# Kernel optimization log

Hardware: AMD Instinct MI355X
Metric: run time of the kernel (lower is better)

The kernel has to match this reference:

```python
import jax, jax.numpy as jnp
import numpy as np

EMBED = 1024
HEADS = 16
HEAD_DIM = EMBED // HEADS  # 64


def setup_inputs() -> dict:
    key = jax.random.key(0)
    k0, k1, k2, k3, k4 = jax.random.split(key, 5)
    scale = 1.0 / np.sqrt(EMBED)
    return {
        "input_tensor": jax.random.normal(k0, (2, 2048, EMBED), dtype=jnp.float32),
        "qkv_w": jax.random.normal(k1, (EMBED, 3 * EMBED), dtype=jnp.float32) * scale,
        "qkv_b": jax.random.normal(k2, (3 * EMBED,), dtype=jnp.float32) * 0.02,
        "out_w": jax.random.normal(k3, (EMBED, EMBED), dtype=jnp.float32) * scale,
        "out_b": jax.random.normal(k4, (EMBED,), dtype=jnp.float32) * 0.02,
    }


def reference(input_tensor, qkv_w, qkv_b, out_w, out_b):
    B, S, _ = input_tensor.shape
    qkv = input_tensor @ qkv_w + qkv_b  # [B,S,3E]
    q, k, v = jnp.split(qkv, 3, axis=-1)
    # [B,S,E] -> [B,H,S,D]
    def to_heads(t):
        return t.reshape(B, S, HEADS, HEAD_DIM).transpose(0, 2, 1, 3)
    q, k, v = to_heads(q), to_heads(k), to_heads(v)
    scores = jnp.einsum("bhqd,bhkd->bhqk", q, k) / jnp.sqrt(jnp.float32(HEAD_DIM))
    probs = jax.nn.softmax(scores, axis=-1)  # dropout p=0 -> identity
    attn = jnp.einsum("bhqk,bhkd->bhqd", probs, v)
    attn = attn.transpose(0, 2, 1, 3).reshape(B, S, EMBED)
    return attn @ out_w + out_b
```

## Files before the change

kernel.cpp:

```cpp
#include <hip/hip_runtime.h>
#include <stdint.h>

typedef short short4v __attribute__((ext_vector_type(4)));
typedef short short8  __attribute__((ext_vector_type(8)));
typedef float f32x4   __attribute__((ext_vector_type(4)));
typedef unsigned int u32x2 __attribute__((ext_vector_type(2)));

#define S_LEN 2048
#define NB    2
#define NH    16
#define HD    64
#define EMB   1024
#define TOK   (NB * S_LEN)
#define QKV_N (3 * EMB)

#define GLD16(gp, lp) __builtin_amdgcn_global_load_lds( \
    (const __attribute__((address_space(1))) void*)(gp), \
    (__attribute__((address_space(3))) void*)(lp), 16, 0, 0)

static __device__ __forceinline__ short f2bf(float f) {
    unsigned int x = __float_as_uint(f);
    unsigned int r = (x + 0x7fffu + ((x >> 16) & 1u)) >> 16;
    return (short)(r & 0xffffu);
}

static __device__ __forceinline__ f32x4 mfma16(short8 a, short8 b, f32x4 c) {
    return __builtin_amdgcn_mfma_f32_16x16x32_bf16(a, b, c, 0, 0, 0);
}

__global__ __launch_bounds__(256) void cvt_f32_bf16(const float* __restrict__ in,
                                                    short* __restrict__ out, int n) {
    int i = (blockIdx.x * 256 + threadIdx.x) * 4;
    if (i < n) {
        float4 v = *reinterpret_cast<const float4*>(in + i);
        short4v o;
        o.x = f2bf(v.x); o.y = f2bf(v.y); o.z = f2bf(v.z); o.w = f2bf(v.w);
        *reinterpret_cast<short4v*>(out + i) = o;
    }
}

__global__ __launch_bounds__(256) void transpose_cvt(const float* __restrict__ w,
                                                     short* __restrict__ wt,
                                                     int K, int N) {
    __shared__ float tile[32][33];
    int tx = threadIdx.x & 31, ty = threadIdx.x >> 5;
    int c0 = blockIdx.x * 32, r0 = blockIdx.y * 32;
    #pragma unroll
    for (int j = 0; j < 4; j++)
        tile[ty + j * 8][tx] = w[(long)(r0 + ty + j * 8) * N + c0 + tx];
    __syncthreads();
    #pragma unroll
    for (int j = 0; j < 4; j++)
        wt[(long)(c0 + ty + j * 8) * K + r0 + tx] = f2bf(tile[tx][ty + j * 8]);
}

__global__ __launch_bounds__(256) void vtrans(const short* __restrict__ v,
                                              short* __restrict__ vt) {
    __shared__ short t[32][33];
    int tx = threadIdx.x & 31, ty = threadIdx.x >> 5;
    int s0 = blockIdx.x * 32, d0 = blockIdx.y * 32, bh = blockIdx.z;
    const long base = (long)bh * S_LEN * HD;
    #pragma unroll
    for (int j = 0; j < 4; j++)
        t[ty + j * 8][tx] = v[base + (long)(s0 + ty + j * 8) * HD + d0 + tx];
    __syncthreads();
    #pragma unroll
    for (int j = 0; j < 4; j++)
        vt[base + (long)(d0 + ty + j * 8) * S_LEN + s0 + tx] = t[tx][ty + j * 8];
}

template <int EPI>
__global__ __launch_bounds__(256) void gemm_bf16(
    const short* __restrict__ A, const short* __restrict__ BT,
    const float* __restrict__ bias,
    short* __restrict__ q_ws, short* __restrict__ k_ws, short* __restrict__ v_ws,
    float* __restrict__ outf, int M, int N, int K) {
    __shared__ __align__(16) short As[128 * 64];
    __shared__ __align__(16) short Bs[128 * 64];
    const int tid = threadIdx.x;
    const int lane = tid & 63, wave = tid >> 6;
    const int wm = wave >> 1, wn = wave & 1;
    const int l15 = lane & 15, lhi = lane >> 4;
    const int bm = blockIdx.y, bn = blockIdx.x;

    const short* gA[4]; const short* gB[4]; short* lA[4]; short* lB[4];
    #pragma unroll
    for (int i = 0; i < 4; i++) {
        int inst = wave * 4 + i;
        int row  = inst * 8 + (lane >> 3);
        int c    = lane & 7, cp = c ^ (row & 7);
        gA[i] = A  + (long)(bm * 128 + row) * K + cp * 8;
        gB[i] = BT + (long)(bn * 128 + row) * K + cp * 8;
        lA[i] = As + inst * 512;
        lB[i] = Bs + inst * 512;
    }

    f32x4 acc[4][4] = {};
    for (int kt = 0; kt < K; kt += 64) {
        #pragma unroll
        for (int i = 0; i < 4; i++) { GLD16(gA[i] + kt, lA[i]); GLD16(gB[i] + kt, lB[i]); }
        __syncthreads();
        #pragma unroll
        for (int ks = 0; ks < 2; ks++) {
            short8 af[4], bfr[4];
            #pragma unroll
            for (int m = 0; m < 4; m++) {
                int row = wm * 64 + m * 16 + l15;
                int cp  = (ks * 4 + lhi) ^ (row & 7);
                af[m] = *(const short8*)(As + row * 64 + cp * 8);
            }
            #pragma unroll
            for (int n = 0; n < 4; n++) {
                int row = wn * 64 + n * 16 + l15;
                int cp  = (ks * 4 + lhi) ^ (row & 7);
                bfr[n] = *(const short8*)(Bs + row * 64 + cp * 8);
            }
            #pragma unroll
            for (int m = 0; m < 4; m++)
                #pragma unroll
                for (int n = 0; n < 4; n++)
                    acc[m][n] = mfma16(af[m], bfr[n], acc[m][n]);
        }
        __syncthreads();
    }

    if (EPI == 0) {
        const int part = bn >> 3;
        short* dst = part == 0 ? q_ws : (part == 1 ? k_ws : v_ws);
        #pragma unroll
        for (int m = 0; m < 4; m++) {
            const int row0 = bm * 128 + wm * 64 + m * 16 + lhi * 4;
            #pragma unroll
            for (int n = 0; n < 4; n++) {
                const int col = bn * 128 + wn * 64 + n * 16 + l15;
                const float bv = bias[col];
                const int nn = col & 1023, h = nn >> 6, d = nn & 63;
                #pragma unroll
                for (int r = 0; r < 4; r++) {
                    const int rr = row0 + r, b = rr >> 11, s = rr & 2047;
                    dst[((long)(b * NH + h) * S_LEN + s) * HD + d] =
                        f2bf(acc[m][n][r] + bv);
                }
            }
        }
    } else {
        #pragma unroll
        for (int m = 0; m < 4; m++) {
            const int row0 = bm * 128 + wm * 64 + m * 16 + lhi * 4;
            #pragma unroll
            for (int n = 0; n < 4; n++) {
                const int col = bn * 128 + wn * 64 + n * 16 + l15;
                const float bv = bias[col];
                #pragma unroll
                for (int r = 0; r < 4; r++)
                    outf[(long)(row0 + r) * N + col] = acc[m][n][r] + bv;
            }
        }
    }
}

__global__ __launch_bounds__(256) void attn_fwd(const short* __restrict__ Qg,
                                                const short* __restrict__ Kg,
                                                const short* __restrict__ Vtg,
                                                short* __restrict__ Og) {
    __shared__ __align__(16) short Ks[64 * 64];
    __shared__ __align__(16) short Vs[64 * 64];
    __shared__ __align__(16) short Pl[4][16][72];
    const int tid = threadIdx.x, lane = tid & 63, wave = tid >> 6;
    const int l15 = lane & 15, lhi = lane >> 4;
    const int bh = blockIdx.y, qt = blockIdx.x;
    const int q0 = qt * 64 + wave * 16;
    const long kbase = (long)bh * S_LEN * HD;
    const long vbase = (long)bh * HD * S_LEN;

    short8 qf[2];
    #pragma unroll
    for (int ks2 = 0; ks2 < 2; ks2++)
        qf[ks2] = *(const short8*)&Qg[kbase + (long)(q0 + l15) * HD + ks2 * 32 + lhi * 8];

    const short* gK[2]; const short* gV[2]; short* lK[2]; short* lV[2];
    #pragma unroll
    for (int i = 0; i < 2; i++) {
        int inst = wave * 2 + i;
        int row  = inst * 8 + (lane >> 3);
        int c    = lane & 7, cp = c ^ (row & 7);
        gK[i] = Kg  + kbase + (long)row * HD + cp * 8;
        gV[i] = Vtg + vbase + (long)row * S_LEN + cp * 8;
        lK[i] = Ks + inst * 512;
        lV[i] = Vs + inst * 512;
    }

    f32x4 accO[4] = {};
    float ms = -1e30f, lp = 0.f;
    const float C2 = 0.18033688f;

    for (int kv = 0; kv < S_LEN; kv += 64) {
        #pragma unroll
        for (int i = 0; i < 2; i++) { GLD16(gK[i] + (long)kv * HD, lK[i]); GLD16(gV[i] + kv, lV[i]); }
        __syncthreads();

        f32x4 accS[4];
        #pragma unroll
        for (int ksub = 0; ksub < 4; ksub++) {
            f32x4 z = {0.f, 0.f, 0.f, 0.f};
            #pragma unroll
            for (int ks2 = 0; ks2 < 2; ks2++) {
                int row = ksub * 16 + l15;
                int cp  = (ks2 * 4 + lhi) ^ (row & 7);
                short8 kf = *(const short8*)(Ks + row * 64 + cp * 8);
                z = mfma16(kf, qf[ks2], z);
            }
            accS[ksub] = z;
        }

        f32x4 mx = accS[0];
        #pragma unroll
        for (int ksub = 1; ksub < 4; ksub++)
            #pragma unroll
            for (int r = 0; r < 4; r++) mx[r] = fmaxf(mx[r], accS[ksub][r]);
        float m4 = fmaxf(fmaxf(mx[0], mx[1]), fmaxf(mx[2], mx[3]));
        m4 = fmaxf(m4, __shfl_xor(m4, 16));
        m4 = fmaxf(m4, __shfl_xor(m4, 32));
        float msc = m4 * C2;

        if (__any(msc > ms + 8.f)) {
            float msn = fmaxf(ms, msc);
            float corr = exp2f(ms - msn);
            ms = msn;
            lp *= corr;
            #pragma unroll
            for (int r = 0; r < 4; r++) {
                float cr = __shfl(corr, lhi * 4 + r);
                #pragma unroll
                for (int ds = 0; ds < 4; ds++) accO[ds][r] *= cr;
            }
        }

        float lsum = 0.f;
        #pragma unroll
        for (int ksub = 0; ksub < 4; ksub++) {
            f32x4 p;
            #pragma unroll
            for (int r = 0; r < 4; r++)
                p[r] = exp2f(fmaf(accS[ksub][r], C2, -ms));
            lsum += (p[0] + p[1]) + (p[2] + p[3]);
            unsigned pa, pb;
            asm("v_cvt_pk_bf16_f32 %0, %1, %2" : "=v"(pa) : "v"(p[0]), "v"(p[1]));
            asm("v_cvt_pk_bf16_f32 %0, %1, %2" : "=v"(pb) : "v"(p[2]), "v"(p[3]));
            u32x2 w; w[0] = pa; w[1] = pb;
            *(u32x2*)(&Pl[wave][l15][ksub * 16 + lhi * 4]) = w;
        }
        lp += lsum;

        #pragma unroll
        for (int ds = 0; ds < 4; ds++) {
            #pragma unroll
            for (int ks2 = 0; ks2 < 2; ks2++) {
                int row = ds * 16 + l15;
                int cp  = (ks2 * 4 + lhi) ^ (row & 7);
                short8 vf = *(const short8*)(Vs + row * 64 + cp * 8);
                short8 pf = *(const short8*)(&Pl[wave][l15][ks2 * 32 + lhi * 8]);
                accO[ds] = mfma16(pf, vf, accO[ds]);
            }
        }
        __syncthreads();
    }

    float L = lp + __shfl_xor(lp, 16);
    L += __shfl_xor(L, 32);
    const int b = bh >> 4, h = bh & 15;
    #pragma unroll
    for (int r = 0; r < 4; r++) {
        float Lr  = __shfl(L, lhi * 4 + r);
        float inv = 1.f / Lr;
        const int s = q0 + lhi * 4 + r;
        #pragma unroll
        for (int ds = 0; ds < 4; ds++)
            Og[((long)(b * S_LEN + s)) * EMB + h * 64 + ds * 16 + l15] =
                f2bf(accO[ds][r] * inv);
    }
}

extern "C" void kernel_launch(void* const* d_in, const int* in_sizes, int n_in,
                              void* d_out, int out_size, void* d_ws, size_t ws_size,
                              hipStream_t stream) {
    const float* x    = (const float*)d_in[0];
    const float* qkvw = (const float*)d_in[1];
    const float* qkvb = (const float*)d_in[2];
    const float* outw = (const float*)d_in[3];
    const float* outb = (const float*)d_in[4];
    float* out = (float*)d_out;

    char* ws = (char*)d_ws;
    size_t off = 0;
    auto alloc = [&](size_t bytes) {
        void* p = ws + off;
        off += (bytes + 255) & ~(size_t)255;
        return p;
    };
    short* xb    = (short*)alloc((size_t)TOK * EMB * 2);
    short* wqkvT = (short*)alloc((size_t)QKV_N * EMB * 2);
    short* owT   = (short*)alloc((size_t)EMB * EMB * 2);
    short* q_ws  = (short*)alloc((size_t)NB * NH * S_LEN * HD * 2);
    short* k_ws  = (short*)alloc((size_t)NB * NH * S_LEN * HD * 2);
    short* v_ws  = (short*)alloc((size_t)NB * NH * S_LEN * HD * 2);
    short* vt_ws = (short*)alloc((size_t)NB * NH * S_LEN * HD * 2);
    short* attn  = (short*)alloc((size_t)TOK * EMB * 2);

    cvt_f32_bf16<<<(TOK * EMB / 4 + 255) / 256, 256, 0, stream>>>(x, xb, TOK * EMB);
    transpose_cvt<<<dim3(QKV_N / 32, EMB / 32), 256, 0, stream>>>(qkvw, wqkvT, EMB, QKV_N);
    transpose_cvt<<<dim3(EMB / 32, EMB / 32), 256, 0, stream>>>(outw, owT, EMB, EMB);

    gemm_bf16<0><<<dim3(QKV_N / 128, TOK / 128), 256, 0, stream>>>(
        xb, wqkvT, qkvb, q_ws, k_ws, v_ws, nullptr, TOK, QKV_N, EMB);

    vtrans<<<dim3(S_LEN / 32, HD / 32, NB * NH), 256, 0, stream>>>(v_ws, vt_ws);

    attn_fwd<<<dim3(S_LEN / 64, NB * NH), 256, 0, stream>>>(q_ws, k_ws, vt_ws, attn);

    gemm_bf16<1><<<dim3(EMB / 128, TOK / 128), 256, 0, stream>>>(
        attn, owT, outb, nullptr, nullptr, nullptr, out, TOK, EMB, EMB);
}
```

Baseline: 231.0 us.

## Double-buffer K/V tiles in attention and swizzle workgroup order

```diff
diff --git a/kernel.cpp b/kernel.cpp
--- a/kernel.cpp
+++ b/kernel.cpp
@@ -163,12 +163,15 @@
                                                 const short* __restrict__ Kg,
                                                 const short* __restrict__ Vtg,
                                                 short* __restrict__ Og) {
-    __shared__ __align__(16) short Ks[64 * 64];
-    __shared__ __align__(16) short Vs[64 * 64];
+    __shared__ __align__(16) short Ks[2][4096];
+    __shared__ __align__(16) short Vs[2][4096];
     __shared__ __align__(16) short Pl[4][16][72];
     const int tid = threadIdx.x, lane = tid & 63, wave = tid >> 6;
     const int l15 = lane & 15, lhi = lane >> 4;
-    const int bh = blockIdx.y, qt = blockIdx.x;
+    const int wg  = blockIdx.x;
+    const int swz = (wg & 7) * 128 + (wg >> 3);
+    const int bh  = swz >> 5;
+    const int qt  = swz & 31;
     const int q0 = qt * 64 + wave * 16;
     const long kbase = (long)bh * S_LEN * HD;
     const long vbase = (long)bh * HD * S_LEN;
@@ -178,46 +181,62 @@
     for (int ks2 = 0; ks2 < 2; ks2++)
         qf[ks2] = *(const short8*)&Qg[kbase + (long)(q0 + l15) * HD + ks2 * 32 + lhi * 8];
 
-    const short* gK[2]; const short* gV[2]; short* lK[2]; short* lV[2];
+    const short* gKp[2]; const short* gVp[2]; int lOff[2];
     #pragma unroll
     for (int i = 0; i < 2; i++) {
         int inst = wave * 2 + i;
         int row  = inst * 8 + (lane >> 3);
-        int c    = lane & 7, cp = c ^ (row & 7);
-        gK[i] = Kg  + kbase + (long)row * HD + cp * 8;
-        gV[i] = Vtg + vbase + (long)row * S_LEN + cp * 8;
-        lK[i] = Ks + inst * 512;
-        lV[i] = Vs + inst * 512;
-    }
+        int cp   = (lane & 7) ^ (row & 7);
+        gKp[i] = Kg  + kbase + (long)row * HD + cp * 8;
+        gVp[i] = Vtg + vbase + (long)row * S_LEN + cp * 8;
+        lOff[i] = inst * 512;
+    }
+
+    int fOff[4][2];
+    #pragma unroll
+    for (int sub = 0; sub < 4; sub++)
+        #pragma unroll
+        for (int ks2 = 0; ks2 < 2; ks2++) {
+            int row = sub * 16 + l15;
+            int cp  = (ks2 * 4 + lhi) ^ (l15 & 7);
+            fOff[sub][ks2] = row * 64 + cp * 8;
+        }
 
     f32x4 accO[4] = {};
     float ms = -1e30f, lp = 0.f;
     const float C2 = 0.18033688f;
 
-    for (int kv = 0; kv < S_LEN; kv += 64) {
-        #pragma unroll
-        for (int i = 0; i < 2; i++) { GLD16(gK[i] + (long)kv * HD, lK[i]); GLD16(gV[i] + kv, lV[i]); }
-        __syncthreads();
-
+    #pragma unroll
+    for (int i = 0; i < 2; i++) { GLD16(gKp[i], &Ks[0][lOff[i]]); GLD16(gVp[i], &Vs[0][lOff[i]]); }
+    __syncthreads();
+
+    const int NT = S_LEN / 64;
+    for (int t = 0; t < NT; t++) {
+        const int cur = t & 1;
+        if (t + 1 < NT) {
+            #pragma unroll
+            for (int i = 0; i < 2; i++) {
+                GLD16(gKp[i] + (long)(t + 1) * 4096, &Ks[cur ^ 1][lOff[i]]);
+                GLD16(gVp[i] + (t + 1) * 64,         &Vs[cur ^ 1][lOff[i]]);
+            }
+        }
         f32x4 accS[4];
         #pragma unroll
-        for (int ksub = 0; ksub < 4; ksub++) {
+        for (int sub = 0; sub < 4; sub++) {
             f32x4 z = {0.f, 0.f, 0.f, 0.f};
             #pragma unroll
             for (int ks2 = 0; ks2 < 2; ks2++) {
-                int row = ksub * 16 + l15;
-                int cp  = (ks2 * 4 + lhi) ^ (row & 7);
-                short8 kf = *(const short8*)(Ks + row * 64 + cp * 8);
+                short8 kf = *(const short8*)&Ks[cur][fOff[sub][ks2]];
                 z = mfma16(kf, qf[ks2], z);
             }
-            accS[ksub] = z;
+            accS[sub] = z;
         }
 
         f32x4 mx = accS[0];
         #pragma unroll
-        for (int ksub = 1; ksub < 4; ksub++)
-            #pragma unroll
-            for (int r = 0; r < 4; r++) mx[r] = fmaxf(mx[r], accS[ksub][r]);
+        for (int sub = 1; sub < 4; sub++)
+            #pragma unroll
+            for (int r = 0; r < 4; r++) mx[r] = fmaxf(mx[r], accS[sub][r]);
         float m4 = fmaxf(fmaxf(mx[0], mx[1]), fmaxf(mx[2], mx[3]));
         m4 = fmaxf(m4, __shfl_xor(m4, 16));
         m4 = fmaxf(m4, __shfl_xor(m4, 32));
@@ -238,30 +257,30 @@
 
         float lsum = 0.f;
         #pragma unroll
-        for (int ksub = 0; ksub < 4; ksub++) {
+        for (int sub = 0; sub < 4; sub++) {
             f32x4 p;
             #pragma unroll
             for (int r = 0; r < 4; r++)
-                p[r] = exp2f(fmaf(accS[ksub][r], C2, -ms));
+                p[r] = exp2f(fmaf(accS[sub][r], C2, -ms));
             lsum += (p[0] + p[1]) + (p[2] + p[3]);
             unsigned pa, pb;
             asm("v_cvt_pk_bf16_f32 %0, %1, %2" : "=v"(pa) : "v"(p[0]), "v"(p[1]));
             asm("v_cvt_pk_bf16_f32 %0, %1, %2" : "=v"(pb) : "v"(p[2]), "v"(p[3]));
             u32x2 w; w[0] = pa; w[1] = pb;
-            *(u32x2*)(&Pl[wave][l15][ksub * 16 + lhi * 4]) = w;
+            *(u32x2*)(&Pl[wave][l15][sub * 16 + lhi * 4]) = w;
         }
         lp += lsum;
 
+        asm volatile("s_waitcnt lgkmcnt(0)" ::: "memory");
+        __builtin_amdgcn_sched_barrier(0);
+        short8 pf0 = *(const short8*)(&Pl[wave][l15][lhi * 8]);
+        short8 pf1 = *(const short8*)(&Pl[wave][l15][32 + lhi * 8]);
         #pragma unroll
         for (int ds = 0; ds < 4; ds++) {
-            #pragma unroll
-            for (int ks2 = 0; ks2 < 2; ks2++) {
-                int row = ds * 16 + l15;
-                int cp  = (ks2 * 4 + lhi) ^ (row & 7);
-                short8 vf = *(const short8*)(Vs + row * 64 + cp * 8);
-                short8 pf = *(const short8*)(&Pl[wave][l15][ks2 * 32 + lhi * 8]);
-                accO[ds] = mfma16(pf, vf, accO[ds]);
-            }
+            short8 vf0 = *(const short8*)&Vs[cur][fOff[ds][0]];
+            short8 vf1 = *(const short8*)&Vs[cur][fOff[ds][1]];
+            accO[ds] = mfma16(pf0, vf0, accO[ds]);
+            accO[ds] = mfma16(pf1, vf1, accO[ds]);
         }
         __syncthreads();
     }
@@ -316,7 +335,7 @@
 
     vtrans<<<dim3(S_LEN / 32, HD / 32, NB * NH), 256, 0, stream>>>(v_ws, vt_ws);
 
-    attn_fwd<<<dim3(S_LEN / 64, NB * NH), 256, 0, stream>>>(q_ws, k_ws, vt_ws, attn);
+    attn_fwd<<<1024, 256, 0, stream>>>(q_ws, k_ws, vt_ws, attn);
 
     gemm_bf16<1><<<dim3(EMB / 128, TOK / 128), 256, 0, stream>>>(
         attn, owT, outb, nullptr, nullptr, nullptr, out, TOK, EMB, EMB);
```

New measurement: 243.6 us. 5.4% more time.
